# Kernel tuning notes

Hardware: AMD Instinct MI355X
Metric: run time of the kernel (lower is better)

Reference implementation:

```python
import jax, jax.numpy as jnp
import numpy as np

B, S, T, K = 128, 4, 16, 36   # questions, answer slots (hardcoded 4), max tags/slot, num boxes
VD, QD, H = 256, 256, 256
NB = B * S * T                # total tag rows = leading dim of v, q


def setup_inputs() -> dict:
    key = jax.random.key(0)
    ks = jax.random.split(key, 8)
    tags_attention = jnp.ones((B, S, T), dtype=jnp.int32)  # all slots full -> sum == NB
    v = jax.random.normal(ks[0], (NB, K, VD), jnp.float32)
    q = jax.random.normal(ks[1], (NB, QD), jnp.float32)
    # binary box mask, first box always valid
    bm = (jax.random.uniform(ks[2], (B, K)) < 0.85).astype(jnp.float32)
    box_mask = bm.at[:, 0].set(1.0)
    Wv = jax.random.normal(ks[3], (H, VD), jnp.float32) / np.sqrt(VD).astype(np.float32)
    bv = jnp.zeros((H,), jnp.float32)
    Wq = jax.random.normal(ks[4], (H, QD), jnp.float32) / np.sqrt(QD).astype(np.float32)
    bq = jnp.zeros((H,), jnp.float32)
    Wl = jax.random.normal(ks[5], (1, H), jnp.float32) / np.sqrt(H).astype(np.float32)
    bl = jnp.zeros((1,), jnp.float32)
    return dict(v=v, q=q, box_mask=box_mask, tags_attention=tags_attention,
                Wv=Wv, bv=bv, Wq=Wq, bq=bq, Wl=Wl, bl=bl)


def reference(v, q, box_mask, tags_attention, Wv, bv, Wq, bq, Wl, bl):
    # FCNet projections (weight-normed Linear + ReLU; dropout inactive at eval)
    v_proj = jax.nn.relu(jnp.einsum('nkd,hd->nkh', v, Wv) + bv)          # [N,K,H]
    q_proj = jax.nn.relu(q @ Wq.T + bq)                                   # [N,H]
    joint = v_proj * q_proj[:, None, :]                                   # [N,K,H]
    logits = jnp.einsum('nkh,h->nk', joint, Wl[0]) + bl[0]                # [N,K]

    # pad_sequence: ragged rows -> [B,S,T,K] via per-slot offsets + masked gather
    Bq, Ss, Tt = tags_attention.shape
    lengths = tags_attention.sum(-1)                                      # [B,S]
    flat_len = lengths.reshape(-1)
    offsets = jnp.concatenate([jnp.zeros((1,), flat_len.dtype),
                               jnp.cumsum(flat_len)[:-1]]).reshape(Bq, Ss)
    t = jnp.arange(Tt)
    idx = offsets[:, :, None] + t                                         # [B,S,T]
    valid = t[None, None, :] < lengths[:, :, None]                        # [B,S,T]
    gathered = logits[jnp.clip(idx, 0, logits.shape[0] - 1)]              # [B,S,T,K]
    logits_batch = jnp.where(valid[..., None], gathered, 0.0)

    # masked_softmax (r2c style): softmax(x*mask)*mask, renormalized
    mask = box_mask[:, None, None, :]                                     # [B,1,1,K]
    w = jax.nn.softmax(logits_batch * mask, axis=-1) * mask
    w = w / (w.sum(-1, keepdims=True) + 1e-13)
    return w
```

## Files before the change

### kernel.cpp

```cpp
#include <hip/hip_runtime.h>
#include <stdint.h>

#define NBROWS 8192
#define KBOX   36
#define MROWS  (NBROWS * KBOX)
#define HDIM   256

typedef __attribute__((ext_vector_type(8))) short bf16x8;
typedef __attribute__((ext_vector_type(4))) float f32x4;

__device__ __forceinline__ unsigned short f2bf(float f) {
  unsigned int u = __float_as_uint(f);
  return (unsigned short)((u + 0x7fffu + ((u >> 16) & 1u)) >> 16);
}

__global__ void cvt_kernel(const float* __restrict__ Wv, const float* __restrict__ Wq,
                           unsigned short* __restrict__ wvb, unsigned short* __restrict__ wqb) {
  int i = blockIdx.x * 256 + threadIdx.x;
  wvb[i] = f2bf(Wv[i]);
  wqb[i] = f2bf(Wq[i]);
}

template<int MODE>
__global__ __launch_bounds__(256, 4)
void gemm_kernel(const float* __restrict__ Amat,
                 const unsigned short* __restrict__ Wbf,
                 const float* __restrict__ bias,
                 const float* __restrict__ wl,
                 const float* __restrict__ g,
                 float* __restrict__ outp,
                 const float* __restrict__ blp)
{
  __shared__ unsigned short Asm[64 * 32];
  __shared__ unsigned short Bsm[256 * 32];
  __shared__ float bias_sm[256];
  __shared__ float aux_sm[4 * 256];
  __shared__ float partial[64 * 4];

  const int t    = threadIdx.x;
  const int lane = t & 63;
  const int wid  = t >> 6;
  const int r0   = blockIdx.x * 64;

  bias_sm[t] = bias[t];
  int n_base = 0;
  if (MODE == 0) {
    aux_sm[t] = wl[t];
  } else {
    n_base = r0 / KBOX;
    #pragma unroll
    for (int i = 0; i < 4; ++i) {
      int idx = t + i * 256;
      int n = n_base + (idx >> 8);
      if (n > NBROWS - 1) n = NBROWS - 1;
      aux_sm[idx] = g[(size_t)n * 256 + (idx & 255)];
    }
  }

  f32x4 acc[4][4];
  #pragma unroll
  for (int a = 0; a < 4; ++a)
    #pragma unroll
    for (int b = 0; b < 4; ++b) acc[a][b] = (f32x4)0.f;

  const int arow = t >> 2;
  const int ako  = t & 3;
  const float* asrc = Amat + (size_t)(r0 + arow) * 256 + ako * 8;
  unsigned short* adst = &Asm[arow * 32 + (ako ^ ((arow >> 1) & 3)) * 8];

  for (int kk = 0; kk < 8; ++kk) {
    const int d0 = kk * 32;
    __syncthreads();
    {
      const float4* s4 = (const float4*)(asrc + d0);
      float4 v0 = s4[0];
      float4 v1 = s4[1];
      uint4 pk;
      pk.x = (unsigned)f2bf(v0.x) | ((unsigned)f2bf(v0.y) << 16);
      pk.y = (unsigned)f2bf(v0.z) | ((unsigned)f2bf(v0.w) << 16);
      pk.z = (unsigned)f2bf(v1.x) | ((unsigned)f2bf(v1.y) << 16);
      pk.w = (unsigned)f2bf(v1.z) | ((unsigned)f2bf(v1.w) << 16);
      *(uint4*)adst = pk;
    }
    #pragma unroll
    for (int i = 0; i < 4; ++i) {
      int u = t + i * 256;
      int brow = u >> 2, bko = u & 3;
      uint4 val = *(const uint4*)&Wbf[brow * 256 + d0 + bko * 8];
      *(uint4*)&Bsm[brow * 32 + (bko ^ ((brow >> 1) & 3)) * 8] = val;
    }
    __syncthreads();
    bf16x8 af[4], bfr[4];
    #pragma unroll
    for (int mf = 0; mf < 4; ++mf) {
      int row  = mf * 16 + (lane & 15);
      int phys = (lane >> 4) ^ ((row >> 1) & 3);
      af[mf] = *(const bf16x8*)&Asm[row * 32 + phys * 8];
    }
    #pragma unroll
    for (int nf = 0; nf < 4; ++nf) {
      int col  = wid * 64 + nf * 16 + (lane & 15);
      int phys = (lane >> 4) ^ ((col >> 1) & 3);
      bfr[nf] = *(const bf16x8*)&Bsm[col * 32 + phys * 8];
    }
    #pragma unroll
    for (int mf = 0; mf < 4; ++mf)
      #pragma unroll
      for (int nf = 0; nf < 4; ++nf)
        acc[mf][nf] = __builtin_amdgcn_mfma_f32_16x16x32_bf16(af[mf], bfr[nf], acc[mf][nf], 0, 0, 0);
  }

  if (MODE == 0) {
    #pragma unroll
    for (int mf = 0; mf < 4; ++mf)
      #pragma unroll
      for (int nf = 0; nf < 4; ++nf) {
        int col = wid * 64 + nf * 16 + (lane & 15);
        float bb = bias_sm[col];
        float ww = aux_sm[col];
        #pragma unroll
        for (int j = 0; j < 4; ++j) {
          int row = mf * 16 + ((lane >> 4) << 2) + j;
          float x = fmaxf(acc[mf][nf][j] + bb, 0.f) * ww;
          outp[(size_t)(r0 + row) * 256 + col] = x;
        }
      }
  } else {
    float s[4][4];
    #pragma unroll
    for (int mf = 0; mf < 4; ++mf) {
      #pragma unroll
      for (int j = 0; j < 4; ++j) {
        int row  = mf * 16 + ((lane >> 4) << 2) + j;
        int nloc = (r0 + row) / KBOX - n_base;
        const float* grow = &aux_sm[nloc * 256];
        float acc_s = 0.f;
        #pragma unroll
        for (int nf = 0; nf < 4; ++nf) {
          int col = wid * 64 + nf * 16 + (lane & 15);
          float x = acc[mf][nf][j] + bias_sm[col];
          acc_s += fmaxf(x, 0.f) * grow[col];
        }
        s[mf][j] = acc_s;
      }
    }
    #pragma unroll
    for (int mf = 0; mf < 4; ++mf)
      #pragma unroll
      for (int j = 0; j < 4; ++j) {
        float vv = s[mf][j];
        vv += __shfl_xor(vv, 1);
        vv += __shfl_xor(vv, 2);
        vv += __shfl_xor(vv, 4);
        vv += __shfl_xor(vv, 8);
        s[mf][j] = vv;
      }
    if ((lane & 15) == 0) {
      #pragma unroll
      for (int mf = 0; mf < 4; ++mf)
        #pragma unroll
        for (int j = 0; j < 4; ++j) {
          int row = mf * 16 + ((lane >> 4) << 2) + j;
          partial[row * 4 + wid] = s[mf][j];
        }
    }
    __syncthreads();
    if (t < 64) {
      float vv = partial[t * 4 + 0] + partial[t * 4 + 1] + partial[t * 4 + 2] + partial[t * 4 + 3];
      outp[r0 + t] = vv + blp[0];
    }
  }
}

__global__ __launch_bounds__(256)
void softmax_kernel(const float* __restrict__ logits, const float* __restrict__ box_mask,
                    float* __restrict__ outp) {
  int n = blockIdx.x * 4 + (threadIdx.x >> 6);
  int k = threadIdx.x & 63;
  int b = n >> 6;
  float l = 0.f, m = 0.f;
  if (k < KBOX) {
    m = box_mask[b * KBOX + k];
    l = logits[(size_t)n * KBOX + k];
  }
  bool act = (k < KBOX) && (m > 0.5f);
  float lm = act ? l : -3.0e38f;
  #pragma unroll
  for (int off = 32; off >= 1; off >>= 1) lm = fmaxf(lm, __shfl_xor(lm, off));
  float e = act ? expf(l - lm) : 0.f;
  float ssum = e;
  #pragma unroll
  for (int off = 32; off >= 1; off >>= 1) ssum += __shfl_xor(ssum, off);
  if (k < KBOX) outp[(size_t)n * KBOX + k] = e / ssum;
}

extern "C" void kernel_launch(void* const* d_in, const int* in_sizes, int n_in,
                              void* d_out, int out_size, void* d_ws, size_t ws_size,
                              hipStream_t stream) {
  const float* v        = (const float*)d_in[0];
  const float* q        = (const float*)d_in[1];
  const float* box_mask = (const float*)d_in[2];
  const float* Wv = (const float*)d_in[4];
  const float* bv = (const float*)d_in[5];
  const float* Wq = (const float*)d_in[6];
  const float* bq = (const float*)d_in[7];
  const float* Wl = (const float*)d_in[8];
  const float* bl = (const float*)d_in[9];
  float* outp = (float*)d_out;

  char* ws = (char*)d_ws;
  unsigned short* wvb = (unsigned short*)ws;
  unsigned short* wqb = (unsigned short*)(ws + 131072);
  float* g      = (float*)(ws + 262144);
  float* logits = (float*)(ws + 262144 + 8388608);

  cvt_kernel<<<256, 256, 0, stream>>>(Wv, Wq, wvb, wqb);
  gemm_kernel<0><<<NBROWS / 64, 256, 0, stream>>>(q, wqb, bq, Wl, nullptr, g, nullptr);
  gemm_kernel<1><<<MROWS / 64, 256, 0, stream>>>(v, wvb, bv, nullptr, g, logits, bl);
  softmax_kernel<<<NBROWS / 4, 256, 0, stream>>>(logits, box_mask, outp);
}
```

Measured before the change: 131.9 us.

## Double-buffer GEMM LDS tiles with async global-to-LDS weight loads and register prefetch

Moves the GEMM K-loop to double-buffered LDS. The weight tile is loaded straight into LDS with global_load_lds, and the fp32 activation rows are prefetched two steps ahead into registers, so loads for the next step overlap the MFMA work of the current one. This drops one barrier per iteration. In exchange it doubles LDS use, raises register pressure, and lowers launch bounds from 4 to 3 blocks per CU, which can reduce occupancy.

```diff
diff --git a/kernel.cpp b/kernel.cpp
--- a/kernel.cpp
+++ b/kernel.cpp
@@ -1,10 +1,10 @@
 #include <hip/hip_runtime.h>
+#include <hip/hip_bf16.h>
 #include <stdint.h>
 
 #define NBROWS 8192
 #define KBOX   36
 #define MROWS  (NBROWS * KBOX)
-#define HDIM   256
 
 typedef __attribute__((ext_vector_type(8))) short bf16x8;
 typedef __attribute__((ext_vector_type(4))) float f32x4;
@@ -12,6 +12,21 @@
 __device__ __forceinline__ unsigned short f2bf(float f) {
   unsigned int u = __float_as_uint(f);
   return (unsigned short)((u + 0x7fffu + ((u >> 16) & 1u)) >> 16);
+}
+
+__device__ __forceinline__ unsigned int pk2(float x, float y) {
+  __hip_bfloat16 hx = __float2bfloat16(x);
+  __hip_bfloat16 hy = __float2bfloat16(y);
+  unsigned short ux, uy;
+  __builtin_memcpy(&ux, &hx, 2);
+  __builtin_memcpy(&uy, &hy, 2);
+  return (unsigned)ux | ((unsigned)uy << 16);
+}
+
+__device__ __forceinline__ void gll16(const void* g, void* l) {
+  __builtin_amdgcn_global_load_lds((const __attribute__((address_space(1))) unsigned int*)g,
+                                   (__attribute__((address_space(3))) unsigned int*)l,
+                                   16, 0, 0);
 }
 
 __global__ void cvt_kernel(const float* __restrict__ Wv, const float* __restrict__ Wq,
@@ -22,7 +37,7 @@
 }
 
 template<int MODE>
-__global__ __launch_bounds__(256, 4)
+__global__ __launch_bounds__(256, 3)
 void gemm_kernel(const float* __restrict__ Amat,
                  const unsigned short* __restrict__ Wbf,
                  const float* __restrict__ bias,
@@ -31,8 +46,8 @@
                  float* __restrict__ outp,
                  const float* __restrict__ blp)
 {
-  __shared__ unsigned short Asm[64 * 32];
-  __shared__ unsigned short Bsm[256 * 32];
+  __shared__ unsigned short Asm[2][64 * 32];
+  __shared__ unsigned short Bsm[2][256 * 32];
   __shared__ float bias_sm[256];
   __shared__ float aux_sm[4 * 256];
   __shared__ float partial[64 * 4];
@@ -57,57 +72,85 @@
     }
   }
 
-  f32x4 acc[4][4];
-  #pragma unroll
-  for (int a = 0; a < 4; ++a)
-    #pragma unroll
-    for (int b = 0; b < 4; ++b) acc[a][b] = (f32x4)0.f;
+  int bh[4], bco[4];
+  #pragma unroll
+  for (int i = 0; i < 4; ++i) {
+    int h = wid * 64 + i * 16 + (lane >> 2);
+    bh[i]  = h;
+    bco[i] = ((lane & 3) ^ ((h >> 1) & 3)) * 8;
+  }
 
   const int arow = t >> 2;
   const int ako  = t & 3;
   const float* asrc = Amat + (size_t)(r0 + arow) * 256 + ako * 8;
-  unsigned short* adst = &Asm[arow * 32 + (ako ^ ((arow >> 1) & 3)) * 8];
-
+  const int adst_off = arow * 32 + (ako ^ ((arow >> 1) & 3)) * 8;
+
+  f32x4 acc[4][4];
+  #pragma unroll
+  for (int a = 0; a < 4; ++a)
+    #pragma unroll
+    for (int b = 0; b < 4; ++b) acc[a][b] = (f32x4)0.f;
+
+  float4 areg[2][2];
+
+  #pragma unroll
+  for (int i = 0; i < 4; ++i)
+    gll16(Wbf + (size_t)bh[i] * 256 + bco[i], &Bsm[0][(wid * 64 + i * 16) * 32]);
+  areg[0][0] = ((const float4*)(asrc + 0))[0];
+  areg[0][1] = ((const float4*)(asrc + 0))[1];
+  areg[1][0] = ((const float4*)(asrc + 32))[0];
+  areg[1][1] = ((const float4*)(asrc + 32))[1];
+  {
+    uint4 pk;
+    pk.x = pk2(areg[0][0].x, areg[0][0].y);
+    pk.y = pk2(areg[0][0].z, areg[0][0].w);
+    pk.z = pk2(areg[0][1].x, areg[0][1].y);
+    pk.w = pk2(areg[0][1].z, areg[0][1].w);
+    *(uint4*)&Asm[0][adst_off] = pk;
+  }
+  __syncthreads();
+
+  #pragma unroll
   for (int kk = 0; kk < 8; ++kk) {
-    const int d0 = kk * 32;
-    __syncthreads();
-    {
-      const float4* s4 = (const float4*)(asrc + d0);
-      float4 v0 = s4[0];
-      float4 v1 = s4[1];
+    const int cur = kk & 1;
+    if (kk < 7) {
+      const int d0 = (kk + 1) * 32;
+      #pragma unroll
+      for (int i = 0; i < 4; ++i)
+        gll16(Wbf + (size_t)bh[i] * 256 + d0 + bco[i], &Bsm[1 - cur][(wid * 64 + i * 16) * 32]);
+      const float4 a0 = areg[(kk + 1) & 1][0];
+      const float4 a1 = areg[(kk + 1) & 1][1];
       uint4 pk;
-      pk.x = (unsigned)f2bf(v0.x) | ((unsigned)f2bf(v0.y) << 16);
-      pk.y = (unsigned)f2bf(v0.z) | ((unsigned)f2bf(v0.w) << 16);
-      pk.z = (unsigned)f2bf(v1.x) | ((unsigned)f2bf(v1.y) << 16);
-      pk.w = (unsigned)f2bf(v1.z) | ((unsigned)f2bf(v1.w) << 16);
-      *(uint4*)adst = pk;
-    }
-    #pragma unroll
-    for (int i = 0; i < 4; ++i) {
-      int u = t + i * 256;
-      int brow = u >> 2, bko = u & 3;
-      uint4 val = *(const uint4*)&Wbf[brow * 256 + d0 + bko * 8];
-      *(uint4*)&Bsm[brow * 32 + (bko ^ ((brow >> 1) & 3)) * 8] = val;
-    }
-    __syncthreads();
+      pk.x = pk2(a0.x, a0.y);
+      pk.y = pk2(a0.z, a0.w);
+      pk.z = pk2(a1.x, a1.y);
+      pk.w = pk2(a1.z, a1.w);
+      *(uint4*)&Asm[1 - cur][adst_off] = pk;
+    }
+    if (kk < 6) {
+      const int d0 = (kk + 2) * 32;
+      areg[kk & 1][0] = ((const float4*)(asrc + d0))[0];
+      areg[kk & 1][1] = ((const float4*)(asrc + d0))[1];
+    }
     bf16x8 af[4], bfr[4];
     #pragma unroll
     for (int mf = 0; mf < 4; ++mf) {
       int row  = mf * 16 + (lane & 15);
       int phys = (lane >> 4) ^ ((row >> 1) & 3);
-      af[mf] = *(const bf16x8*)&Asm[row * 32 + phys * 8];
+      af[mf] = *(const bf16x8*)&Asm[cur][row * 32 + phys * 8];
     }
     #pragma unroll
     for (int nf = 0; nf < 4; ++nf) {
       int col  = wid * 64 + nf * 16 + (lane & 15);
       int phys = (lane >> 4) ^ ((col >> 1) & 3);
-      bfr[nf] = *(const bf16x8*)&Bsm[col * 32 + phys * 8];
+      bfr[nf] = *(const bf16x8*)&Bsm[cur][col * 32 + phys * 8];
     }
     #pragma unroll
     for (int mf = 0; mf < 4; ++mf)
       #pragma unroll
       for (int nf = 0; nf < 4; ++nf)
         acc[mf][nf] = __builtin_amdgcn_mfma_f32_16x16x32_bf16(af[mf], bfr[nf], acc[mf][nf], 0, 0, 0);
+    __syncthreads();
   }
 
   if (MODE == 0) {
```

New measurement: 121.6 us. -7.8%, faster.

## Persistent streaming GEMM with LDS-resident weights and fused softmax

Applied to the files above, without the earlier changes.

Replaces the tiled GEMM kernels with persistent blocks that load the full bf16 weight matrix into LDS once via global_load_lds, then stream 32-row chunks of activations straight from global memory into registers with double buffering. The v-projection kernel now also runs the masked softmax from LDS-held logits, which removes the separate softmax launch and the logits round-trip. Each block holds 128KB of LDS and runs at one block per CU, so latency hiding depends entirely on the register double buffering. Only 256 blocks are launched for the main pass.

```diff
diff --git a/kernel.cpp b/kernel.cpp
--- a/kernel.cpp
+++ b/kernel.cpp
@@ -1,10 +1,10 @@
 #include <hip/hip_runtime.h>
+#include <hip/hip_bf16.h>
 #include <stdint.h>
 
 #define NBROWS 8192
 #define KBOX   36
 #define MROWS  (NBROWS * KBOX)
-#define HDIM   256
 
 typedef __attribute__((ext_vector_type(8))) short bf16x8;
 typedef __attribute__((ext_vector_type(4))) float f32x4;
@@ -12,6 +12,21 @@
 __device__ __forceinline__ unsigned short f2bf(float f) {
   unsigned int u = __float_as_uint(f);
   return (unsigned short)((u + 0x7fffu + ((u >> 16) & 1u)) >> 16);
+}
+
+__device__ __forceinline__ unsigned int pk2(float x, float y) {
+  __hip_bfloat16 hx = __float2bfloat16(x);
+  __hip_bfloat16 hy = __float2bfloat16(y);
+  unsigned short ux, uy;
+  __builtin_memcpy(&ux, &hx, 2);
+  __builtin_memcpy(&uy, &hy, 2);
+  return (unsigned)ux | ((unsigned)uy << 16);
+}
+
+__device__ __forceinline__ void gll16(const void* g, void* l) {
+  __builtin_amdgcn_global_load_lds((const __attribute__((address_space(1))) unsigned int*)g,
+                                   (__attribute__((address_space(3))) unsigned int*)l,
+                                   16, 0, 0);
 }
 
 __global__ void cvt_kernel(const float* __restrict__ Wv, const float* __restrict__ Wq,
@@ -21,177 +36,180 @@
   wqb[i] = f2bf(Wq[i]);
 }
 
-template<int MODE>
-__global__ __launch_bounds__(256, 4)
-void gemm_kernel(const float* __restrict__ Amat,
-                 const unsigned short* __restrict__ Wbf,
-                 const float* __restrict__ bias,
-                 const float* __restrict__ wl,
-                 const float* __restrict__ g,
-                 float* __restrict__ outp,
-                 const float* __restrict__ blp)
+template<int MODE, int NCHUNK>
+__global__ __launch_bounds__(256, 1)
+void stream_kernel(const float* __restrict__ Amat,
+                   const unsigned short* __restrict__ Wbf,
+                   const float* __restrict__ bias,
+                   const float* __restrict__ wl,
+                   const float* __restrict__ g,
+                   const float* __restrict__ blp,
+                   const float* __restrict__ bmask,
+                   float* __restrict__ outp)
 {
-  __shared__ unsigned short Asm[64 * 32];
-  __shared__ unsigned short Bsm[256 * 32];
-  __shared__ float bias_sm[256];
-  __shared__ float aux_sm[4 * 256];
-  __shared__ float partial[64 * 4];
+  __shared__ unsigned short Wlds[256 * 256];
+  __shared__ float part[2][32][4];
+  __shared__ float logit_sm[NCHUNK * 32 >= KBOX ? NCHUNK * 32 : KBOX];
 
   const int t    = threadIdx.x;
   const int lane = t & 63;
   const int wid  = t >> 6;
-  const int r0   = blockIdx.x * 64;
-
-  bias_sm[t] = bias[t];
-  int n_base = 0;
-  if (MODE == 0) {
-    aux_sm[t] = wl[t];
-  } else {
-    n_base = r0 / KBOX;
-    #pragma unroll
-    for (int i = 0; i < 4; ++i) {
-      int idx = t + i * 256;
-      int n = n_base + (idx >> 8);
-      if (n > NBROWS - 1) n = NBROWS - 1;
-      aux_sm[idx] = g[(size_t)n * 256 + (idx & 255)];
-    }
-  }
-
-  f32x4 acc[4][4];
+  const int l15  = lane & 15;
+  const int lq   = lane >> 4;
+  const long long row_base = (long long)blockIdx.x * (NCHUNK * 32);
+
+  {
+    const int cadd = lane >> 5;
+    const int p    = lane & 31;
+    #pragma unroll
+    for (int i = 0; i < 32; ++i) {
+      int colbase = wid * 64 + i * 2;
+      int col = colbase + cadd;
+      gll16(Wbf + col * 256 + (p ^ (col & 7)) * 8, &Wlds[colbase * 256]);
+    }
+  }
+
+  float breg[4], wlg[4];
   #pragma unroll
-  for (int a = 0; a < 4; ++a)
-    #pragma unroll
-    for (int b = 0; b < 4; ++b) acc[a][b] = (f32x4)0.f;
-
-  const int arow = t >> 2;
-  const int ako  = t & 3;
-  const float* asrc = Amat + (size_t)(r0 + arow) * 256 + ako * 8;
-  unsigned short* adst = &Asm[arow * 32 + (ako ^ ((arow >> 1) & 3)) * 8];
-
-  for (int kk = 0; kk < 8; ++kk) {
-    const int d0 = kk * 32;
-    __syncthreads();
-    {
-      const float4* s4 = (const float4*)(asrc + d0);
-      float4 v0 = s4[0];
-      float4 v1 = s4[1];
-      uint4 pk;
-      pk.x = (unsigned)f2bf(v0.x) | ((unsigned)f2bf(v0.y) << 16);
-      pk.y = (unsigned)f2bf(v0.z) | ((unsigned)f2bf(v0.w) << 16);
-      pk.z = (unsigned)f2bf(v1.x) | ((unsigned)f2bf(v1.y) << 16);
-      pk.w = (unsigned)f2bf(v1.z) | ((unsigned)f2bf(v1.w) << 16);
-      *(uint4*)adst = pk;
-    }
-    #pragma unroll
-    for (int i = 0; i < 4; ++i) {
-      int u = t + i * 256;
-      int brow = u >> 2, bko = u & 3;
-      uint4 val = *(const uint4*)&Wbf[brow * 256 + d0 + bko * 8];
-      *(uint4*)&Bsm[brow * 32 + (bko ^ ((brow >> 1) & 3)) * 8] = val;
-    }
-    __syncthreads();
-    bf16x8 af[4], bfr[4];
-    #pragma unroll
-    for (int mf = 0; mf < 4; ++mf) {
-      int row  = mf * 16 + (lane & 15);
-      int phys = (lane >> 4) ^ ((row >> 1) & 3);
-      af[mf] = *(const bf16x8*)&Asm[row * 32 + phys * 8];
-    }
-    #pragma unroll
-    for (int nf = 0; nf < 4; ++nf) {
-      int col  = wid * 64 + nf * 16 + (lane & 15);
-      int phys = (lane >> 4) ^ ((col >> 1) & 3);
-      bfr[nf] = *(const bf16x8*)&Bsm[col * 32 + phys * 8];
-    }
-    #pragma unroll
-    for (int mf = 0; mf < 4; ++mf)
-      #pragma unroll
-      for (int nf = 0; nf < 4; ++nf)
-        acc[mf][nf] = __builtin_amdgcn_mfma_f32_16x16x32_bf16(af[mf], bfr[nf], acc[mf][nf], 0, 0, 0);
-  }
-
-  if (MODE == 0) {
-    #pragma unroll
-    for (int mf = 0; mf < 4; ++mf)
+  for (int nf = 0; nf < 4; ++nf) {
+    int col = wid * 64 + nf * 16 + l15;
+    breg[nf] = bias[col];
+    wlg[nf]  = (MODE == 0) ? wl[col] : 0.f;
+  }
+  const float blv = (MODE == 1) ? blp[0] : 0.f;
+
+  float4 bufA[2][8][2], bufB[2][8][2];
+  float gA0[4], gA1[4], gB0[4], gB1[4];
+
+  auto issueA = [&](int c, float4 (&buf)[2][8][2], float (&g0)[4], float (&g1)[4]) {
+    if (c >= NCHUNK) return;
+    const float* src = Amat + (row_base + c * 32) * 256;
+    #pragma unroll
+    for (int m = 0; m < 2; ++m)
+      #pragma unroll
+      for (int kk = 0; kk < 8; ++kk) {
+        const float* p = src + (m * 16 + l15) * 256 + kk * 32 + lq * 8;
+        buf[m][kk][0] = ((const float4*)p)[0];
+        buf[m][kk][1] = ((const float4*)p)[1];
+      }
+    if (MODE == 1) {
+      int m0 = (int)row_base + c * 32;
+      int n0 = m0 / KBOX;
+      int n1 = (m0 + 31) / KBOX;
       #pragma unroll
       for (int nf = 0; nf < 4; ++nf) {
-        int col = wid * 64 + nf * 16 + (lane & 15);
-        float bb = bias_sm[col];
-        float ww = aux_sm[col];
+        int col = wid * 64 + nf * 16 + l15;
+        g0[nf] = g[n0 * 256 + col];
+        g1[nf] = g[n1 * 256 + col];
+      }
+    }
+  };
+
+  auto compute = [&](int c, float4 (&buf)[2][8][2], float (&g0)[4], float (&g1)[4]) {
+    f32x4 acc[2][4];
+    #pragma unroll
+    for (int m = 0; m < 2; ++m)
+      #pragma unroll
+      for (int nf = 0; nf < 4; ++nf) acc[m][nf] = (f32x4)0.f;
+
+    #pragma unroll
+    for (int kk = 0; kk < 8; ++kk) {
+      bf16x8 bfr[4];
+      #pragma unroll
+      for (int nf = 0; nf < 4; ++nf) {
+        int col = wid * 64 + nf * 16 + l15;
+        int pc  = (kk * 4 + lq) ^ (col & 7);
+        bfr[nf] = *(const bf16x8*)&Wlds[col * 256 + pc * 8];
+      }
+      #pragma unroll
+      for (int m = 0; m < 2; ++m) {
+        float4 a0 = buf[m][kk][0], a1 = buf[m][kk][1];
+        uint4 pk;
+        pk.x = pk2(a0.x, a0.y); pk.y = pk2(a0.z, a0.w);
+        pk.z = pk2(a1.x, a1.y); pk.w = pk2(a1.z, a1.w);
+        bf16x8 af;
+        __builtin_memcpy(&af, &pk, 16);
+        #pragma unroll
+        for (int nf = 0; nf < 4; ++nf)
+          acc[m][nf] = __builtin_amdgcn_mfma_f32_16x16x32_bf16(af, bfr[nf], acc[m][nf], 0, 0, 0);
+      }
+    }
+
+    if (MODE == 0) {
+      #pragma unroll
+      for (int m = 0; m < 2; ++m)
+        #pragma unroll
+        for (int nf = 0; nf < 4; ++nf) {
+          int col = wid * 64 + nf * 16 + l15;
+          #pragma unroll
+          for (int j = 0; j < 4; ++j) {
+            long long row = row_base + c * 32 + m * 16 + lq * 4 + j;
+            outp[row * 256 + col] = fmaxf(acc[m][nf][j] + breg[nf], 0.f) * wlg[nf];
+          }
+        }
+    } else {
+      int m0  = (int)row_base + c * 32;
+      int bnd = (m0 / KBOX + 1) * KBOX - m0;
+      #pragma unroll
+      for (int m = 0; m < 2; ++m)
         #pragma unroll
         for (int j = 0; j < 4; ++j) {
-          int row = mf * 16 + ((lane >> 4) << 2) + j;
-          float x = fmaxf(acc[mf][nf][j] + bb, 0.f) * ww;
-          outp[(size_t)(r0 + row) * 256 + col] = x;
+          int rloc = m * 16 + lq * 4 + j;
+          float s = 0.f;
+          #pragma unroll
+          for (int nf = 0; nf < 4; ++nf) {
+            float gv = (rloc >= bnd) ? g1[nf] : g0[nf];
+            s += fmaxf(acc[m][nf][j] + breg[nf], 0.f) * gv;
+          }
+          s += __shfl_xor(s, 1);
+          s += __shfl_xor(s, 2);
+          s += __shfl_xor(s, 4);
+          s += __shfl_xor(s, 8);
+          if (l15 == 0) part[c & 1][rloc][wid] = s;
         }
-      }
-  } else {
-    float s[4][4];
-    #pragma unroll
-    for (int mf = 0; mf < 4; ++mf) {
-      #pragma unroll
-      for (int j = 0; j < 4; ++j) {
-        int row  = mf * 16 + ((lane >> 4) << 2) + j;
-        int nloc = (r0 + row) / KBOX - n_base;
-        const float* grow = &aux_sm[nloc * 256];
-        float acc_s = 0.f;
-        #pragma unroll
-        for (int nf = 0; nf < 4; ++nf) {
-          int col = wid * 64 + nf * 16 + (lane & 15);
-          float x = acc[mf][nf][j] + bias_sm[col];
-          acc_s += fmaxf(x, 0.f) * grow[col];
-        }
-        s[mf][j] = acc_s;
-      }
-    }
-    #pragma unroll
-    for (int mf = 0; mf < 4; ++mf)
-      #pragma unroll
-      for (int j = 0; j < 4; ++j) {
-        float vv = s[mf][j];
-        vv += __shfl_xor(vv, 1);
-        vv += __shfl_xor(vv, 2);
-        vv += __shfl_xor(vv, 4);
-        vv += __shfl_xor(vv, 8);
-        s[mf][j] = vv;
-      }
-    if ((lane & 15) == 0) {
-      #pragma unroll
-      for (int mf = 0; mf < 4; ++mf)
-        #pragma unroll
-        for (int j = 0; j < 4; ++j) {
-          int row = mf * 16 + ((lane >> 4) << 2) + j;
-          partial[row * 4 + wid] = s[mf][j];
-        }
-    }
+      __syncthreads();
+      if (lane < 8) {
+        int r = wid * 8 + lane;
+        logit_sm[c * 32 + r] = part[c & 1][r][0] + part[c & 1][r][1]
+                             + part[c & 1][r][2] + part[c & 1][r][3] + blv;
+      }
+    }
+  };
+
+  issueA(0, bufA, gA0, gA1);
+  __syncthreads();
+
+  #pragma unroll 1
+  for (int cpair = 0; cpair < NCHUNK / 2; ++cpair) {
+    issueA(2 * cpair + 1, bufB, gB0, gB1);
+    compute(2 * cpair, bufA, gA0, gA1);
+    issueA(2 * cpair + 2, bufA, gA0, gA1);
+    compute(2 * cpair + 1, bufB, gB0, gB1);
+  }
+
+  if (MODE == 1) {
     __syncthreads();
-    if (t < 64) {
-      float vv = partial[t * 4 + 0] + partial[t * 4 + 1] + partial[t * 4 + 2] + partial[t * 4 + 3];
-      outp[r0 + t] = vv + blp[0];
-    }
-  }
-}
-
-__global__ __launch_bounds__(256)
-void softmax_kernel(const float* __restrict__ logits, const float* __restrict__ box_mask,
-                    float* __restrict__ outp) {
-  int n = blockIdx.x * 4 + (threadIdx.x >> 6);
-  int k = threadIdx.x & 63;
-  int b = n >> 6;
-  float l = 0.f, m = 0.f;
-  if (k < KBOX) {
-    m = box_mask[b * KBOX + k];
-    l = logits[(size_t)n * KBOX + k];
-  }
-  bool act = (k < KBOX) && (m > 0.5f);
-  float lm = act ? l : -3.0e38f;
-  #pragma unroll
-  for (int off = 32; off >= 1; off >>= 1) lm = fmaxf(lm, __shfl_xor(lm, off));
-  float e = act ? expf(l - lm) : 0.f;
-  float ssum = e;
-  #pragma unroll
-  for (int off = 32; off >= 1; off >>= 1) ssum += __shfl_xor(ssum, off);
-  if (k < KBOX) outp[(size_t)n * KBOX + k] = e / ssum;
+    #pragma unroll 1
+    for (int bb = 0; bb < 8; ++bb) {
+      int box = wid * 8 + bb;
+      long long boxg = (long long)blockIdx.x * 32 + box;
+      int bidx = (int)(boxg >> 6);
+      float mk = 0.f, lv = 0.f;
+      if (lane < KBOX) {
+        mk = bmask[bidx * KBOX + lane];
+        lv = logit_sm[box * KBOX + lane];
+      }
+      bool act = (lane < KBOX) && (mk > 0.5f);
+      float lm = act ? lv : -3.0e38f;
+      #pragma unroll
+      for (int off = 32; off >= 1; off >>= 1) lm = fmaxf(lm, __shfl_xor(lm, off));
+      float e = act ? expf(lv - lm) : 0.f;
+      float ssum = e;
+      #pragma unroll
+      for (int off = 32; off >= 1; off >>= 1) ssum += __shfl_xor(ssum, off);
+      if (lane < KBOX) outp[boxg * KBOX + lane] = e / ssum;
+    }
+  }
 }
 
 extern "C" void kernel_launch(void* const* d_in, const int* in_sizes, int n_in,
@@ -211,11 +229,9 @@
   char* ws = (char*)d_ws;
   unsigned short* wvb = (unsigned short*)ws;
   unsigned short* wqb = (unsigned short*)(ws + 131072);
-  float* g      = (float*)(ws + 262144);
-  float* logits = (float*)(ws + 262144 + 8388608);
+  float* g = (float*)(ws + 262144);
 
   cvt_kernel<<<256, 256, 0, stream>>>(Wv, Wq, wvb, wqb);
-  gemm_kernel<0><<<NBROWS / 64, 256, 0, stream>>>(q, wqb, bq, Wl, nullptr, g, nullptr);
-  gemm_kernel<1><<<MROWS / 64, 256, 0, stream>>>(v, wvb, bv, nullptr, g, logits, bl);
-  softmax_kernel<<<NBROWS / 4, 256, 0, stream>>>(logits, box_mask, outp);
-}
+  stream_kernel<0, 2><<<128, 256, 0, stream>>>(q, wqb, bq, Wl, nullptr, nullptr, nullptr, g);
+  stream_kernel<1, 36><<<256, 256, 0, stream>>>(v, wvb, bv, nullptr, g, bl, box_mask, outp);
+}
```

After: 235.2 us. +78.3%, slower.

## Restructure GEMM: full-K A tile in LDS, B fragments streamed from global with prefetch

Applied to the files above, without the earlier changes.

The GEMM is rewritten to load the whole 256-wide A row tile into LDS once, converted to bf16 with an XOR swizzle. B fragments are read directly from global or L2 into registers with double-buffered prefetch, replacing the per-k-step LDS staging and its two barriers per iteration. Blocks grow to 512 threads arranged as 8 waves in a 2x4 layout. Bias and Wl move into registers, and the shuffle reduction is folded into the epilogue. This cuts LDS traffic and synchronisation, but each wave now fetches B from global memory itself, which puts more load on the cache.

```diff
diff --git a/kernel.cpp b/kernel.cpp
--- a/kernel.cpp
+++ b/kernel.cpp
@@ -1,10 +1,10 @@
 #include <hip/hip_runtime.h>
+#include <hip/hip_bf16.h>
 #include <stdint.h>
 
 #define NBROWS 8192
 #define KBOX   36
 #define MROWS  (NBROWS * KBOX)
-#define HDIM   256
 
 typedef __attribute__((ext_vector_type(8))) short bf16x8;
 typedef __attribute__((ext_vector_type(4))) float f32x4;
@@ -12,6 +12,15 @@
 __device__ __forceinline__ unsigned short f2bf(float f) {
   unsigned int u = __float_as_uint(f);
   return (unsigned short)((u + 0x7fffu + ((u >> 16) & 1u)) >> 16);
+}
+
+__device__ __forceinline__ unsigned int pk2(float x, float y) {
+  __hip_bfloat16 hx = __float2bfloat16(x);
+  __hip_bfloat16 hy = __float2bfloat16(y);
+  unsigned short ux, uy;
+  __builtin_memcpy(&ux, &hx, 2);
+  __builtin_memcpy(&uy, &hy, 2);
+  return (unsigned)ux | ((unsigned)uy << 16);
 }
 
 __global__ void cvt_kernel(const float* __restrict__ Wv, const float* __restrict__ Wq,
@@ -22,154 +31,151 @@
 }
 
 template<int MODE>
-__global__ __launch_bounds__(256, 4)
-void gemm_kernel(const float* __restrict__ Amat,
-                 const unsigned short* __restrict__ Wbf,
-                 const float* __restrict__ bias,
-                 const float* __restrict__ wl,
-                 const float* __restrict__ g,
-                 float* __restrict__ outp,
-                 const float* __restrict__ blp)
+__global__ __launch_bounds__(512, 4)
+void gemm2_kernel(const float* __restrict__ Amat,
+                  const unsigned short* __restrict__ Wbf,
+                  const float* __restrict__ bias,
+                  const float* __restrict__ wl,
+                  const float* __restrict__ g,
+                  const float* __restrict__ blp,
+                  float* __restrict__ outp)
 {
-  __shared__ unsigned short Asm[64 * 32];
-  __shared__ unsigned short Bsm[256 * 32];
-  __shared__ float bias_sm[256];
-  __shared__ float aux_sm[4 * 256];
-  __shared__ float partial[64 * 4];
+  constexpr int BM = MODE ? 64 : 32;
+  constexpr int MF = MODE ? 2 : 1;
+  constexpr int RW = BM / 8;
+
+  __shared__ unsigned short Asm[BM * 256];
+  __shared__ float gtile[MODE ? 3 * 256 : 4];
+  __shared__ float partial[MODE ? 64 * 4 : 4];
 
   const int t    = threadIdx.x;
   const int lane = t & 63;
   const int wid  = t >> 6;
-  const int r0   = blockIdx.x * 64;
-
-  bias_sm[t] = bias[t];
-  int n_base = 0;
+  const int wn   = wid & 3;
+  const int wm   = wid >> 2;
+  const int l15  = lane & 15;
+  const int lq   = lane >> 4;
+  const int r0   = blockIdx.x * BM;
+
+  int n0 = 0;
+  if (MODE == 1) {
+    n0 = r0 / KBOX;
+    int n = n0 + (t >> 8);
+    if (n > NBROWS - 1) n = NBROWS - 1;
+    gtile[t] = g[(size_t)n * 256 + (t & 255)];
+    if (t < 256) {
+      int n2 = n0 + 2;
+      if (n2 > NBROWS - 1) n2 = NBROWS - 1;
+      gtile[512 + t] = g[(size_t)n2 * 256 + t];
+    }
+  }
+
+  float bias_r[4], wl_r[4];
+  #pragma unroll
+  for (int nf = 0; nf < 4; ++nf) {
+    int col = wn * 64 + nf * 16 + l15;
+    bias_r[nf] = bias[col];
+    wl_r[nf]   = (MODE == 0) ? wl[col] : 0.f;
+  }
+  const float blv = (MODE == 1) ? blp[0] : 0.f;
+
+  {
+    float4 st[RW];
+    const float* base = Amat + (size_t)(r0 + wid * RW) * 256 + lane * 4;
+    #pragma unroll
+    for (int i = 0; i < RW; ++i) st[i] = *(const float4*)(base + i * 256);
+    #pragma unroll
+    for (int i = 0; i < RW; ++i) {
+      int r = wid * RW + i;
+      uint2 w;
+      w.x = pk2(st[i].x, st[i].y);
+      w.y = pk2(st[i].z, st[i].w);
+      *(uint2*)&Asm[r * 256 + (((lane >> 1) ^ (r & 7)) << 3) + ((lane & 1) << 2)] = w;
+    }
+  }
+
+  uint4 bA[4], bB[4];
+  #define LOADB(kk, b)                                                              \
+    _Pragma("unroll")                                                               \
+    for (int nf = 0; nf < 4; ++nf)                                                  \
+      b[nf] = *(const uint4*)&Wbf[(size_t)(wn * 64 + nf * 16 + l15) * 256 + (kk) * 32 + lq * 8];
+  LOADB(0, bA);
+  __syncthreads();
+
+  f32x4 acc[MF][4];
+  #pragma unroll
+  for (int mf = 0; mf < MF; ++mf)
+    #pragma unroll
+    for (int nf = 0; nf < 4; ++nf) acc[mf][nf] = (f32x4)0.f;
+
+  #define STEP(kk, bc, bn, prefetch)                                                \
+    do {                                                                            \
+      if (prefetch) { LOADB((kk) + 1, bn); }                                        \
+      bf16x8 af[MF];                                                                \
+      _Pragma("unroll")                                                             \
+      for (int mf = 0; mf < MF; ++mf) {                                             \
+        int row = wm * (16 * MF) + mf * 16 + l15;                                   \
+        af[mf] = *(const bf16x8*)&Asm[row * 256 + ((((kk) * 4 + lq) ^ (row & 7)) << 3)]; \
+      }                                                                             \
+      _Pragma("unroll")                                                             \
+      for (int mf = 0; mf < MF; ++mf)                                               \
+        _Pragma("unroll")                                                           \
+        for (int nf = 0; nf < 4; ++nf) {                                            \
+          bf16x8 bb;                                                                \
+          __builtin_memcpy(&bb, &bc[nf], 16);                                       \
+          acc[mf][nf] = __builtin_amdgcn_mfma_f32_16x16x32_bf16(af[mf], bb, acc[mf][nf], 0, 0, 0); \
+        }                                                                           \
+    } while (0)
+
+  STEP(0, bA, bB, true);
+  STEP(1, bB, bA, true);
+  STEP(2, bA, bB, true);
+  STEP(3, bB, bA, true);
+  STEP(4, bA, bB, true);
+  STEP(5, bB, bA, true);
+  STEP(6, bA, bB, true);
+  STEP(7, bB, bA, false);
+
   if (MODE == 0) {
-    aux_sm[t] = wl[t];
-  } else {
-    n_base = r0 / KBOX;
-    #pragma unroll
-    for (int i = 0; i < 4; ++i) {
-      int idx = t + i * 256;
-      int n = n_base + (idx >> 8);
-      if (n > NBROWS - 1) n = NBROWS - 1;
-      aux_sm[idx] = g[(size_t)n * 256 + (idx & 255)];
-    }
-  }
-
-  f32x4 acc[4][4];
-  #pragma unroll
-  for (int a = 0; a < 4; ++a)
-    #pragma unroll
-    for (int b = 0; b < 4; ++b) acc[a][b] = (f32x4)0.f;
-
-  const int arow = t >> 2;
-  const int ako  = t & 3;
-  const float* asrc = Amat + (size_t)(r0 + arow) * 256 + ako * 8;
-  unsigned short* adst = &Asm[arow * 32 + (ako ^ ((arow >> 1) & 3)) * 8];
-
-  for (int kk = 0; kk < 8; ++kk) {
-    const int d0 = kk * 32;
-    __syncthreads();
-    {
-      const float4* s4 = (const float4*)(asrc + d0);
-      float4 v0 = s4[0];
-      float4 v1 = s4[1];
-      uint4 pk;
-      pk.x = (unsigned)f2bf(v0.x) | ((unsigned)f2bf(v0.y) << 16);
-      pk.y = (unsigned)f2bf(v0.z) | ((unsigned)f2bf(v0.w) << 16);
-      pk.z = (unsigned)f2bf(v1.x) | ((unsigned)f2bf(v1.y) << 16);
-      pk.w = (unsigned)f2bf(v1.z) | ((unsigned)f2bf(v1.w) << 16);
-      *(uint4*)adst = pk;
-    }
-    #pragma unroll
-    for (int i = 0; i < 4; ++i) {
-      int u = t + i * 256;
-      int brow = u >> 2, bko = u & 3;
-      uint4 val = *(const uint4*)&Wbf[brow * 256 + d0 + bko * 8];
-      *(uint4*)&Bsm[brow * 32 + (bko ^ ((brow >> 1) & 3)) * 8] = val;
-    }
-    __syncthreads();
-    bf16x8 af[4], bfr[4];
-    #pragma unroll
-    for (int mf = 0; mf < 4; ++mf) {
-      int row  = mf * 16 + (lane & 15);
-      int phys = (lane >> 4) ^ ((row >> 1) & 3);
-      af[mf] = *(const bf16x8*)&Asm[row * 32 + phys * 8];
-    }
-    #pragma unroll
-    for (int nf = 0; nf < 4; ++nf) {
-      int col  = wid * 64 + nf * 16 + (lane & 15);
-      int phys = (lane >> 4) ^ ((col >> 1) & 3);
-      bfr[nf] = *(const bf16x8*)&Bsm[col * 32 + phys * 8];
-    }
-    #pragma unroll
-    for (int mf = 0; mf < 4; ++mf)
-      #pragma unroll
-      for (int nf = 0; nf < 4; ++nf)
-        acc[mf][nf] = __builtin_amdgcn_mfma_f32_16x16x32_bf16(af[mf], bfr[nf], acc[mf][nf], 0, 0, 0);
-  }
-
-  if (MODE == 0) {
-    #pragma unroll
-    for (int mf = 0; mf < 4; ++mf)
+    #pragma unroll
+    for (int mf = 0; mf < MF; ++mf)
       #pragma unroll
       for (int nf = 0; nf < 4; ++nf) {
-        int col = wid * 64 + nf * 16 + (lane & 15);
-        float bb = bias_sm[col];
-        float ww = aux_sm[col];
+        int col = wn * 64 + nf * 16 + l15;
         #pragma unroll
         for (int j = 0; j < 4; ++j) {
-          int row = mf * 16 + ((lane >> 4) << 2) + j;
-          float x = fmaxf(acc[mf][nf][j] + bb, 0.f) * ww;
-          outp[(size_t)(r0 + row) * 256 + col] = x;
+          int row = r0 + wm * (16 * MF) + mf * 16 + lq * 4 + j;
+          outp[(size_t)row * 256 + col] = fmaxf(acc[mf][nf][j] + bias_r[nf], 0.f) * wl_r[nf];
         }
       }
   } else {
-    float s[4][4];
-    #pragma unroll
-    for (int mf = 0; mf < 4; ++mf) {
+    #pragma unroll
+    for (int mf = 0; mf < MF; ++mf)
       #pragma unroll
       for (int j = 0; j < 4; ++j) {
-        int row  = mf * 16 + ((lane >> 4) << 2) + j;
-        int nloc = (r0 + row) / KBOX - n_base;
-        const float* grow = &aux_sm[nloc * 256];
-        float acc_s = 0.f;
+        int rloc = wm * (16 * MF) + mf * 16 + lq * 4 + j;
+        int nl   = (r0 + rloc) / KBOX - n0;
+        const float* grow = &gtile[nl * 256];
+        float sv = 0.f;
         #pragma unroll
         for (int nf = 0; nf < 4; ++nf) {
-          int col = wid * 64 + nf * 16 + (lane & 15);
-          float x = acc[mf][nf][j] + bias_sm[col];
-          acc_s += fmaxf(x, 0.f) * grow[col];
+          int col = wn * 64 + nf * 16 + l15;
+          sv += fmaxf(acc[mf][nf][j] + bias_r[nf], 0.f) * grow[col];
         }
-        s[mf][j] = acc_s;
+        sv += __shfl_xor(sv, 1);
+        sv += __shfl_xor(sv, 2);
+        sv += __shfl_xor(sv, 4);
+        sv += __shfl_xor(sv, 8);
+        if (l15 == 0) partial[rloc * 4 + wn] = sv;
       }
-    }
-    #pragma unroll
-    for (int mf = 0; mf < 4; ++mf)
-      #pragma unroll
-      for (int j = 0; j < 4; ++j) {
-        float vv = s[mf][j];
-        vv += __shfl_xor(vv, 1);
-        vv += __shfl_xor(vv, 2);
-        vv += __shfl_xor(vv, 4);
-        vv += __shfl_xor(vv, 8);
-        s[mf][j] = vv;
-      }
-    if ((lane & 15) == 0) {
-      #pragma unroll
-      for (int mf = 0; mf < 4; ++mf)
-        #pragma unroll
-        for (int j = 0; j < 4; ++j) {
-          int row = mf * 16 + ((lane >> 4) << 2) + j;
-          partial[row * 4 + wid] = s[mf][j];
-        }
-    }
     __syncthreads();
     if (t < 64) {
-      float vv = partial[t * 4 + 0] + partial[t * 4 + 1] + partial[t * 4 + 2] + partial[t * 4 + 3];
-      outp[r0 + t] = vv + blp[0];
+      outp[r0 + t] = partial[t * 4 + 0] + partial[t * 4 + 1]
+                   + partial[t * 4 + 2] + partial[t * 4 + 3] + blv;
     }
   }
+  #undef STEP
+  #undef LOADB
 }
 
 __global__ __launch_bounds__(256)
@@ -215,7 +221,7 @@
   float* logits = (float*)(ws + 262144 + 8388608);
 
   cvt_kernel<<<256, 256, 0, stream>>>(Wv, Wq, wvb, wqb);
-  gemm_kernel<0><<<NBROWS / 64, 256, 0, stream>>>(q, wqb, bq, Wl, nullptr, g, nullptr);
-  gemm_kernel<1><<<MROWS / 64, 256, 0, stream>>>(v, wvb, bv, nullptr, g, logits, bl);
+  gemm2_kernel<0><<<NBROWS / 32, 512, 0, stream>>>(q, wqb, bq, Wl, nullptr, nullptr, g);
+  gemm2_kernel<1><<<MROWS / 64, 512, 0, stream>>>(v, wvb, bv, nullptr, g, bl, logits);
   softmax_kernel<<<NBROWS / 4, 256, 0, stream>>>(logits, box_mask, outp);
 }
```

Result: slower. 182.5 us (+38.3%).
